# Performance work log

Hardware: AMD Instinct MI355X
Metric: run time of the kernel (lower is better)

The kernel has to match this reference:

```python
import jax, jax.numpy as jnp
import numpy as np


def setup_inputs() -> dict:
    key = jax.random.key(0)
    k1, k2, k3, k4, k5, k6 = jax.random.split(key, 6)
    B, T, U, D, V = 4, 512, 128, 512, 512
    speech = jax.random.normal(k1, (B, T, D), dtype=jnp.float32)
    text = jax.random.normal(k2, (B, U, D), dtype=jnp.float32)
    W = jax.random.normal(k3, (V, D), dtype=jnp.float32) / np.sqrt(D)
    b = jax.random.normal(k4, (V,), dtype=jnp.float32) * 0.01
    speech_len = jax.random.randint(k5, (B,), 1, T + 1, dtype=jnp.int32)
    text_len = jax.random.randint(k6, (B,), 1, U + 1, dtype=jnp.int32)
    return {"speech": speech, "text": text, "W": W, "b": b,
            "speech_len": speech_len, "text_len": text_len}


def reference(speech, text, W, b, speech_len, text_len):
    # RNN-T joint network: broadcast-add encoder and predictor outputs,
    # then project to vocab. speech: [B,T,D], text: [B,U,D].
    joint = speech[:, :, None, :] + text[:, None, :, :]       # [B,T,U,D]
    logits = jnp.einsum('btud,vd->btuv', joint, W) + b         # [B,T,U,V]
    return logits, speech_len, text_len
```

## Files before the change

kernel.cpp:

```cpp
#include <hip/hip_runtime.h>

#define B_ 4
#define T_ 512
#define U_ 128
#define D_ 512
#define V_ 512
#define MS (B_ * T_)
#define MT (B_ * U_)
#define MTOT (MS + MT)
#define LOGITS_ELEMS ((size_t)B_ * T_ * U_ * V_)

#define TM 128
#define TN 64
#define TK 32
#define XSTR 132
#define WSTR 68

#define S_ELEMS ((size_t)MS * V_)
#define TX_ELEMS ((size_t)MT * V_)
#define PSTRIDE (S_ELEMS + TX_ELEMS)

typedef float f32x4 __attribute__((ext_vector_type(4)));

__global__ __launch_bounds__(256, 2) void gemm_joint(
    const float* __restrict__ speech, const float* __restrict__ text,
    const float* __restrict__ W, const float* __restrict__ bias,
    float* __restrict__ S, float* __restrict__ Tx, int ktiles)
{
    __shared__ float Xt[TK][XSTR];
    __shared__ float Wt[TK][WSTR];

    const int tid = threadIdx.x;
    const int m0 = blockIdx.x * TM;
    const int n0 = blockIdx.y * TN;
    const int z  = blockIdx.z;
    const int kbase = z * ktiles * TK;
    const int tx = tid & 15;
    const int ty = tid >> 4;

    S  += (size_t)z * PSTRIDE;
    Tx += (size_t)z * PSTRIDE;

    const float* xbase = (m0 < MS) ? (speech + (size_t)m0 * D_)
                                   : (text + (size_t)(m0 - MS) * D_);

    float acc[8][4] = {};
    float4 xr[4], wr[2];

    #pragma unroll
    for (int i = 0; i < 4; ++i) {
        const int q = tid + 256 * i;
        xr[i] = *(const float4*)(xbase + (size_t)(q >> 3) * D_ + kbase + ((q & 7) << 2));
    }
    #pragma unroll
    for (int i = 0; i < 2; ++i) {
        const int q = tid + 256 * i;
        wr[i] = *(const float4*)(W + (size_t)(n0 + (q >> 3)) * D_ + kbase + ((q & 7) << 2));
    }
    #pragma unroll
    for (int i = 0; i < 4; ++i) {
        const int q = tid + 256 * i;
        const int r = q >> 3, c = (q & 7) << 2;
        Xt[c + 0][r] = xr[i].x; Xt[c + 1][r] = xr[i].y;
        Xt[c + 2][r] = xr[i].z; Xt[c + 3][r] = xr[i].w;
    }
    #pragma unroll
    for (int i = 0; i < 2; ++i) {
        const int q = tid + 256 * i;
        const int r = q >> 3, c = (q & 7) << 2;
        Wt[c + 0][r] = wr[i].x; Wt[c + 1][r] = wr[i].y;
        Wt[c + 2][r] = wr[i].z; Wt[c + 3][r] = wr[i].w;
    }
    __syncthreads();

    for (int t = 0; t < ktiles; ++t) {
        if (t + 1 < ktiles) {
            const int kn = kbase + (t + 1) * TK;
            #pragma unroll
            for (int i = 0; i < 4; ++i) {
                const int q = tid + 256 * i;
                xr[i] = *(const float4*)(xbase + (size_t)(q >> 3) * D_ + kn + ((q & 7) << 2));
            }
            #pragma unroll
            for (int i = 0; i < 2; ++i) {
                const int q = tid + 256 * i;
                wr[i] = *(const float4*)(W + (size_t)(n0 + (q >> 3)) * D_ + kn + ((q & 7) << 2));
            }
        }

        #pragma unroll 8
        for (int k = 0; k < TK; ++k) {
            const float4 a0 = *(const float4*)&Xt[k][ty * 8];
            const float4 a1 = *(const float4*)&Xt[k][ty * 8 + 4];
            const float4 b0 = *(const float4*)&Wt[k][tx * 4];
            const float av[8] = {a0.x, a0.y, a0.z, a0.w, a1.x, a1.y, a1.z, a1.w};
            const float bv[4] = {b0.x, b0.y, b0.z, b0.w};
            #pragma unroll
            for (int i = 0; i < 8; ++i)
                #pragma unroll
                for (int j = 0; j < 4; ++j)
                    acc[i][j] += av[i] * bv[j];
        }

        if (t + 1 < ktiles) {
            __syncthreads();
            #pragma unroll
            for (int i = 0; i < 4; ++i) {
                const int q = tid + 256 * i;
                const int r = q >> 3, c = (q & 7) << 2;
                Xt[c + 0][r] = xr[i].x; Xt[c + 1][r] = xr[i].y;
                Xt[c + 2][r] = xr[i].z; Xt[c + 3][r] = xr[i].w;
            }
            #pragma unroll
            for (int i = 0; i < 2; ++i) {
                const int q = tid + 256 * i;
                const int r = q >> 3, c = (q & 7) << 2;
                Wt[c + 0][r] = wr[i].x; Wt[c + 1][r] = wr[i].y;
                Wt[c + 2][r] = wr[i].z; Wt[c + 3][r] = wr[i].w;
            }
            __syncthreads();
        }
    }

    const int vbase = n0 + tx * 4;
    #pragma unroll
    for (int i = 0; i < 8; ++i) {
        const int m = m0 + ty * 8 + i;
        float4 o;
        o.x = acc[i][0]; o.y = acc[i][1]; o.z = acc[i][2]; o.w = acc[i][3];
        if (m < MS) {
            *(float4*)(S + (size_t)m * V_ + vbase) = o;
        } else {
            if (kbase == 0) {
                o.x += bias[vbase + 0];
                o.y += bias[vbase + 1];
                o.z += bias[vbase + 2];
                o.w += bias[vbase + 3];
            }
            *(float4*)(Tx + (size_t)(m - MS) * V_ + vbase) = o;
        }
    }
}

template <bool SPLIT>
__global__ __launch_bounds__(256, 8) void bcast_add(
    const float* __restrict__ S, const float* __restrict__ Tx,
    const int* __restrict__ sl, const int* __restrict__ tl,
    float* __restrict__ out)
{
    const int V4 = V_ / 4;
    const int bt = blockIdx.x;
    const int b  = bt >> 9;
    const int tid = threadIdx.x;

    if (bt == 0 && tid < 2 * B_) {
        out[LOGITS_ELEMS + tid] = (tid < B_) ? (float)sl[tid]
                                             : (float)tl[tid - B_];
    }

    const f32x4* S4 = (const f32x4*)S + (size_t)bt * V4;
    const f32x4* T4 = (const f32x4*)Tx + (size_t)b * U_ * V4;
    f32x4* O4 = (f32x4*)out + (size_t)bt * U_ * V4;

    f32x4 sv = S4[tid & (V4 - 1)];
    if (SPLIT) sv += S4[(PSTRIDE / 4) + (tid & (V4 - 1))];

    #pragma unroll 8
    for (int idx = tid; idx < U_ * V4; idx += 256) {
        f32x4 tv = T4[idx];
        if (SPLIT) tv += T4[(PSTRIDE / 4) + idx];
        __builtin_nontemporal_store(sv + tv, &O4[idx]);
    }
}

extern "C" void kernel_launch(void* const* d_in, const int* in_sizes, int n_in,
                              void* d_out, int out_size, void* d_ws, size_t ws_size,
                              hipStream_t stream) {
    const float* speech = (const float*)d_in[0];
    const float* text   = (const float*)d_in[1];
    const float* W      = (const float*)d_in[2];
    const float* bias   = (const float*)d_in[3];
    const int*   sl     = (const int*)d_in[4];
    const int*   tl     = (const int*)d_in[5];
    float* out = (float*)d_out;

    float* S  = (float*)d_ws;
    float* Tx = S + S_ELEMS;

    const bool split = ws_size >= 2 * PSTRIDE * sizeof(float);

    if (split) {
        dim3 g1(MTOT / TM, V_ / TN, 2);
        gemm_joint<<<g1, 256, 0, stream>>>(speech, text, W, bias, S, Tx, (D_ / TK) / 2);
        bcast_add<true><<<MS, 256, 0, stream>>>(S, Tx, sl, tl, out);
    } else {
        dim3 g1(MTOT / TM, V_ / TN, 1);
        gemm_joint<<<g1, 256, 0, stream>>>(speech, text, W, bias, S, Tx, D_ / TK);
        bcast_add<false><<<MS, 256, 0, stream>>>(S, Tx, sl, tl, out);
    }
}
```

Measured before the change: 561.0 us.

## Tile broadcast-add over T and U chunks to reuse loaded text rows

The broadcast-add kernel now tiles its grid by (T chunk of 16, U chunk of 32, batch), keeps 16 speech rows in registers and reuses each loaded text vector for 16 output rows. This cuts the redundant reads of the text projection, which were repeated for every time step. Stores also switch from nontemporal to regular writes, and launch bounds drop to 2 blocks per SM to make room for the larger register footprint. The output write stream, about 537 MB, still dominates, so the gain depends on reduced read traffic and on how the cache handles regular stores.

```diff
diff --git a/kernel.cpp b/kernel.cpp
--- a/kernel.cpp
+++ b/kernel.cpp
@@ -19,6 +19,11 @@
 #define S_ELEMS ((size_t)MS * V_)
 #define TX_ELEMS ((size_t)MT * V_)
 #define PSTRIDE (S_ELEMS + TX_ELEMS)
+#define PS4 (PSTRIDE / 4)
+
+#define TCH 16
+#define UCH 32
+#define V4_ (V_ / 4)
 
 typedef float f32x4 __attribute__((ext_vector_type(4)));
 
@@ -143,33 +148,43 @@
 }
 
 template <bool SPLIT>
-__global__ __launch_bounds__(256, 8) void bcast_add(
+__global__ __launch_bounds__(256, 2) void bcast_add(
     const float* __restrict__ S, const float* __restrict__ Tx,
     const int* __restrict__ sl, const int* __restrict__ tl,
     float* __restrict__ out)
 {
-    const int V4 = V_ / 4;
-    const int bt = blockIdx.x;
-    const int b  = bt >> 9;
     const int tid = threadIdx.x;
-
-    if (bt == 0 && tid < 2 * B_) {
+    const int tc = blockIdx.x;
+    const int uq = blockIdx.y;
+    const int b  = blockIdx.z;
+    const int t0 = tc * TCH;
+    const int u0 = uq * UCH;
+
+    if ((tc | uq | b) == 0 && tid < 2 * B_) {
         out[LOGITS_ELEMS + tid] = (tid < B_) ? (float)sl[tid]
                                              : (float)tl[tid - B_];
     }
 
-    const f32x4* S4 = (const f32x4*)S + (size_t)bt * V4;
-    const f32x4* T4 = (const f32x4*)Tx + (size_t)b * U_ * V4;
-    f32x4* O4 = (f32x4*)out + (size_t)bt * U_ * V4;
-
-    f32x4 sv = S4[tid & (V4 - 1)];
-    if (SPLIT) sv += S4[(PSTRIDE / 4) + (tid & (V4 - 1))];
-
-    #pragma unroll 8
-    for (int idx = tid; idx < U_ * V4; idx += 256) {
+    const f32x4* S4 = (const f32x4*)S;
+    const f32x4* T4 = (const f32x4*)Tx + ((size_t)b * U_ + u0) * V4_;
+    f32x4* O4 = (f32x4*)out + (((size_t)b * T_ + t0) * U_ + u0) * V4_;
+
+    const int v4 = tid & (V4_ - 1);
+    f32x4 sv[TCH];
+    #pragma unroll
+    for (int t = 0; t < TCH; ++t) {
+        const size_t si = ((size_t)b * T_ + t0 + t) * V4_ + v4;
+        sv[t] = S4[si];
+        if (SPLIT) sv[t] += S4[PS4 + si];
+    }
+
+    #pragma unroll 2
+    for (int idx = tid; idx < UCH * V4_; idx += 256) {
         f32x4 tv = T4[idx];
-        if (SPLIT) tv += T4[(PSTRIDE / 4) + idx];
-        __builtin_nontemporal_store(sv + tv, &O4[idx]);
+        if (SPLIT) tv += T4[PS4 + idx];
+        #pragma unroll
+        for (int t = 0; t < TCH; ++t)
+            O4[(size_t)t * (U_ * V4_) + idx] = sv[t] + tv;
     }
 }
 
@@ -188,14 +203,15 @@
     float* Tx = S + S_ELEMS;
 
     const bool split = ws_size >= 2 * PSTRIDE * sizeof(float);
+    dim3 g2(T_ / TCH, U_ / UCH, B_);
 
     if (split) {
         dim3 g1(MTOT / TM, V_ / TN, 2);
         gemm_joint<<<g1, 256, 0, stream>>>(speech, text, W, bias, S, Tx, (D_ / TK) / 2);
-        bcast_add<true><<<MS, 256, 0, stream>>>(S, Tx, sl, tl, out);
+        bcast_add<true><<<g2, 256, 0, stream>>>(S, Tx, sl, tl, out);
     } else {
         dim3 g1(MTOT / TM, V_ / TN, 1);
         gemm_joint<<<g1, 256, 0, stream>>>(speech, text, W, bias, S, Tx, D_ / TK);
-        bcast_add<false><<<MS, 256, 0, stream>>>(S, Tx, sl, tl, out);
+        bcast_add<false><<<g2, 256, 0, stream>>>(S, Tx, sl, tl, out);
     }
 }
```

Result: slower. 591.4 us (+5.4%).
